# Performance work log

Hardware: AMD Instinct MI355X
Metric: run time of the kernel (lower is better)

The kernel has to match this reference:

```python
import jax, jax.numpy as jnp
import numpy as np

N, F, H, T = 8192, 64, 64, 64   # nodes, fea_hid, gcn_hid, trans_hid
E = 262144                       # edges (avg degree 32)
S, K = 128, 128                  # subgraphs, subgraph size
NEG = 4                          # neg_num


def prelu(x, a):
    return jnp.where(x >= 0, x, a * x)


def setup_inputs() -> dict:
    key = jax.random.key(0)
    ks = jax.random.split(key, 20)
    inp = {}
    inp["feat"] = jax.random.normal(ks[0], (N, F), jnp.float32)
    inp["edge_src"] = jax.random.randint(ks[1], (E,), 0, N)
    inp["edge_dst"] = jax.random.randint(ks[2], (E,), 0, N)
    inp["edge_w"] = jax.random.uniform(ks[3], (E,), jnp.float32)   # normalized adj values
    inp["avg_w"] = jax.random.uniform(ks[4], (E,), jnp.float32)    # adj_avg values
    inp["neg_idx1"] = jax.random.randint(ks[5], (NEG, N), 0, N)
    inp["neg_idx2"] = jax.random.randint(ks[6], (NEG, N), 0, N)
    inp["a_subg_idx"] = jax.random.randint(ks[7], (S, K), 0, N)
    inp["n_subg_idx"] = jax.random.randint(ks[8], (S, K), 0, N)
    inp["a_lap"] = jax.random.normal(ks[9], (S, K, K), jnp.float32) * 0.1
    inp["n_lap"] = jax.random.normal(ks[10], (S, K, K), jnp.float32) * 0.1
    sc = lambda k, sh, d: jax.random.normal(k, sh, jnp.float32) / np.float32(np.sqrt(d))
    inp["W1"] = sc(ks[11], (F, H), F); inp["b1"] = jnp.zeros((H,), jnp.float32)
    inp["W2"] = sc(ks[12], (H, H), H); inp["b2"] = jnp.zeros((H,), jnp.float32)
    inp["Wq"] = sc(ks[13], (H, T), H); inp["bq"] = jnp.zeros((T,), jnp.float32)
    inp["Ws"] = sc(ks[14], (T, 1), T); inp["bs"] = jnp.zeros((1,), jnp.float32)
    inp["B1"] = sc(ks[15], (F, T), F); inp["bd1"] = jnp.zeros((), jnp.float32)
    inp["B2"] = sc(ks[16], (T, H), T); inp["bd2"] = jnp.zeros((), jnp.float32)
    inp["a1"] = jnp.full((), 0.25, jnp.float32)  # PReLU slopes
    inp["a2"] = jnp.full((), 0.25, jnp.float32)
    inp["aq"] = jnp.full((), 0.25, jnp.float32)
    return inp


def _agg(h, src, dst, w):
    # sparse matmul: (sparse adj) @ h via gather + segment_sum
    return jax.ops.segment_sum(w[:, None] * h[src], dst, num_segments=N)


def _forward(feat, edge_w, avg_w, a_lap, n_lap, W1, b1, W2, b2, Wq, bq, Ws, bs,
             B1, bd1, B2, bd2, a1, a2, aq,
             edge_src, edge_dst, neg_idx1, neg_idx2, a_subg_idx, n_subg_idx):
    # GCN 1: fc -> spmm -> +bias -> PReLU ; node_transemb = pre-propagation features
    h1 = feat @ W1                                             # [N,H]  node_transemb
    v1 = prelu(_agg(h1, edge_src, edge_dst, edge_w) + b1, a1)  # [N,H]
    # GCN 2
    h2 = v1 @ W2
    v2 = prelu(_agg(h2, edge_src, edge_dst, edge_w) + b2, a2)
    # transq + PReLU
    node_vec = prelu(v2 @ Wq + bq, aq)                          # [N,T]
    # AvgNeighbor on node_transemb
    node_neighbor = _agg(h1, edge_src, edge_dst, avg_w)         # [N,H]
    # Discriminator 1: bilinear(feat, node_vec); negatives shuffle feat
    p1 = jnp.einsum('nf,ft,nt->n', feat, B1, node_vec) + bd1    # [N]
    n1 = jnp.einsum('knf,ft,nt->kn', feat[neg_idx1], B1, node_vec) + bd1  # [NEG,N]
    # Discriminator 2: bilinear(node_vec, node_neighbor); negatives shuffle node_vec
    p2 = jnp.einsum('nt,th,nh->n', node_vec, B2, node_neighbor) + bd2
    n2 = jnp.einsum('knt,th,nh->kn', node_vec[neg_idx2], B2, node_neighbor) + bd2
    # MIL scores
    score = jax.nn.sigmoid(node_vec @ Ws + bs)[:, 0]            # [N]
    # batched subgraph losses (replaces ragged python loop)
    a_s = score[a_subg_idx]                                     # [S,K]
    n_s = score[n_subg_idx]                                     # [S,K]
    hom = (jnp.einsum('sk,skj,sj->s', a_s, a_lap, a_s)
           + jnp.einsum('sk,skj,sj->s', n_s, n_lap, n_s))       # [S]
    a_sort = -jnp.sort(-a_s, axis=1)                            # descending sort
    n_sort = -jnp.sort(-n_s, axis=1)
    # first position with value below the subgraph mean
    avg_idx = jnp.argmax(a_sort < jnp.mean(a_sort, axis=1, keepdims=True), axis=1)  # [S]
    a_at_avg = jnp.take_along_axis(a_sort, avg_idx[:, None], axis=1)[:, 0]
    ranking_loss = jnp.mean(jax.nn.relu(1.0 - a_sort[:, 0] + n_sort[:, 0]))
    ranking_inner_loss = jnp.mean(jax.nn.relu(1.0 - a_sort[:, 0] + a_at_avg))
    sp_loss = jnp.mean(jnp.sum(a_s, axis=1))
    hom_loss = jnp.sum(hom) / (2.0 * S)
    adj_rebuilt = jax.nn.sigmoid(node_vec @ node_vec.T)         # [N,N]
    return (ranking_loss, ranking_inner_loss, sp_loss, hom_loss, adj_rebuilt,
            p1, n1, p2, n2)


def reference(feat, edge_src, edge_dst, edge_w, avg_w, neg_idx1, neg_idx2,
              a_subg_idx, n_subg_idx, a_lap, n_lap,
              W1, b1, W2, b2, Wq, bq, Ws, bs, B1, bd1, B2, bd2, a1, a2, aq):
    return _forward(feat, edge_w, avg_w, a_lap, n_lap, W1, b1, W2, b2, Wq, bq, Ws, bs,
                    B1, bd1, B2, bd2, a1, a2, aq,
                    edge_src, edge_dst, neg_idx1, neg_idx2, a_subg_idx, n_subg_idx)
```

## Files before the change

### kernel.cpp

```cpp
#include <hip/hip_runtime.h>

#define Nn 8192
#define Ee 262144
#define NEGk 4

#define OFF_H1   0u
#define OFF_M1   524288u
#define OFF_V1   1048576u
#define OFF_NN   1572864u
#define OFF_H2   2097152u
#define OFF_V2   2621440u
#define OFF_NV   3145728u
#define OFF_M2   3670016u
#define OFF_SC   4194304u
#define OFF_PR   4202496u
#define OFF_PI   4202624u
#define OFF_PS   4202752u
#define OFF_PH   4202880u
#define OFF_CNT  4203008u
#define OFF_CUR  4211200u
#define OFF_RS   4219392u
#define OFF_ESRC 4227600u
#define OFF_EW   4489744u
#define OFF_EAW  4751888u
#define OFF_NVH  5014032u
#define OFF_NVL  5276176u
#define OFF_WT   5538320u

using short8 = __attribute__((ext_vector_type(8))) short;
using f32x4  = __attribute__((ext_vector_type(4))) float;

__device__ inline float wave_sum(float v){
  #pragma unroll
  for (int o = 32; o > 0; o >>= 1) v += __shfl_down(v, o, 64);
  return v;
}
__device__ inline float wave_max(float v){
  #pragma unroll
  for (int o = 32; o > 0; o >>= 1) v = fmaxf(v, __shfl_down(v, o, 64));
  return v;
}
__device__ inline unsigned short f2bf(float x){
  unsigned u = __float_as_uint(x);
  unsigned r = (u + 0x7FFFu + ((u >> 16) & 1u)) >> 16;
  return (unsigned short)r;
}
__device__ inline float bf2f(unsigned short h){ return __uint_as_float(((unsigned)h) << 16); }

__global__ __launch_bounds__(256) void zero_k(int* cnt, int* cur){
  int i = blockIdx.x * 256 + threadIdx.x;
  cnt[i] = 0; cur[i] = 0;
}

__global__ __launch_bounds__(256) void hist_k(const int* __restrict__ dst, int* __restrict__ cnt){
  int e = blockIdx.x * 256 + threadIdx.x;
  atomicAdd(&cnt[dst[e]], 1);
}

__global__ __launch_bounds__(256) void scan_k(const int* __restrict__ cnt, int* __restrict__ rs){
  __shared__ int part[256];
  int tid = threadIdx.x;
  int base = tid * 32;
  int local[32]; int s = 0;
  #pragma unroll
  for (int i = 0; i < 32; i++){ local[i] = s; s += cnt[base + i]; }
  part[tid] = s; __syncthreads();
  for (int off = 1; off < 256; off <<= 1){
    int v = (tid >= off) ? part[tid - off] : 0;
    __syncthreads();
    part[tid] += v;
    __syncthreads();
  }
  int ex = part[tid] - s;
  #pragma unroll
  for (int i = 0; i < 32; i++) rs[base + i] = ex + local[i];
  if (tid == 255) rs[Nn] = part[255];
}

__global__ __launch_bounds__(256) void scatter_k(const int* __restrict__ dst, const int* __restrict__ src,
    const float* __restrict__ ew, const float* __restrict__ aw,
    const int* __restrict__ rs, int* __restrict__ cur,
    int* __restrict__ cs, float* __restrict__ cw, float* __restrict__ caw){
  int e = blockIdx.x * 256 + threadIdx.x;
  int d = dst[e];
  int pos = atomicAdd(&cur[d], 1);
  int j = rs[d] + pos;
  cs[j] = src[e]; cw[j] = ew[e]; caw[j] = aw[e];
}

__global__ __launch_bounds__(256) void wtrans_k(const float* __restrict__ W1, const float* __restrict__ B1,
    const float* __restrict__ W2, const float* __restrict__ Wq, const float* __restrict__ B2,
    float* __restrict__ Wt){
  int idx = blockIdx.x * 256 + threadIdx.x;
  int m = idx >> 12, rc = idx & 4095;
  int k = rc >> 6, c = rc & 63;
  const float* src = (m == 0) ? W1 : (m == 1) ? B1 : (m == 2) ? W2 : (m == 3) ? Wq : B2;
  Wt[m * 4096 + c * 64 + k] = src[k * 64 + c];
}

template<bool DUAL, bool EPI, bool BF>
__global__ __launch_bounds__(256) void fc2_k(const float* __restrict__ X,
    const float* __restrict__ WtA, const float* __restrict__ WtB,
    const float* __restrict__ bias, const float* __restrict__ alpha,
    float* __restrict__ Ya, float* __restrict__ Yb,
    unsigned short* __restrict__ hi, unsigned short* __restrict__ lo){
  __shared__ float As[32 * 68];
  int tid = threadIdx.x;
  int r0 = blockIdx.x * 32;
  for (int i = tid; i < 512; i += 256){
    int r = i >> 4, kq = (i & 15) << 2;
    *(float4*)(As + r * 68 + kq) = *(const float4*)(X + (r0 + r) * 64 + kq);
  }
  __syncthreads();
  int tx = tid & 63, wv = tid >> 6;
  float acca[8], accb[8];
  #pragma unroll
  for (int r = 0; r < 8; r++){ acca[r] = 0.f; accb[r] = 0.f; }
  const float* wpa = WtA + tx * 64;
  const float* wpb = DUAL ? (WtB + tx * 64) : WtA;
  #pragma unroll 4
  for (int kq = 0; kq < 64; kq += 4){
    float4 w = *(const float4*)(wpa + kq);
    float4 w2 = *(const float4*)(wpb + kq);
    #pragma unroll
    for (int r = 0; r < 8; r++){
      float4 a = *(const float4*)(As + (wv * 8 + r) * 68 + kq);
      acca[r] += a.x * w.x + a.y * w.y + a.z * w.z + a.w * w.w;
      if (DUAL) accb[r] += a.x * w2.x + a.y * w2.y + a.z * w2.z + a.w * w2.w;
    }
  }
  float al = EPI ? alpha[0] : 0.f;
  float bi = EPI ? bias[tx] : 0.f;
  #pragma unroll
  for (int r = 0; r < 8; r++){
    int row = r0 + wv * 8 + r;
    float x = acca[r];
    if (EPI){ x += bi; x = (x >= 0.f) ? x : al * x; }
    Ya[row * 64 + tx] = x;
    if (BF){
      unsigned short h = f2bf(x);
      hi[row * 64 + tx] = h;
      lo[row * 64 + tx] = f2bf(x - bf2f(h));
    }
    if (DUAL) Yb[row * 64 + tx] = accb[r];
  }
}

template<bool DUAL>
__global__ __launch_bounds__(256) void agg_k(const float* __restrict__ h,
    const int* __restrict__ rs, const int* __restrict__ cs,
    const float* __restrict__ cw, const float* __restrict__ caw,
    const float* __restrict__ bias, const float* __restrict__ alpha,
    float* __restrict__ out1, float* __restrict__ out2){
  int node = (blockIdx.x << 2) + (threadIdx.x >> 6);
  int lane = threadIdx.x & 63;
  int s = rs[node], e = rs[node + 1];
  float acc = 0.f, acc2 = 0.f;
  int i = s;
  for (; i + 4 <= e; i += 4){
    int s0 = cs[i], s1 = cs[i+1], s2 = cs[i+2], s3 = cs[i+3];
    float w0 = cw[i], w1 = cw[i+1], w2 = cw[i+2], w3 = cw[i+3];
    float h0 = h[(s0 << 6) + lane];
    float h1v = h[(s1 << 6) + lane];
    float h2v = h[(s2 << 6) + lane];
    float h3 = h[(s3 << 6) + lane];
    acc += w0 * h0 + w1 * h1v + w2 * h2v + w3 * h3;
    if (DUAL){
      float a0 = caw[i], a1 = caw[i+1], a2 = caw[i+2], a3 = caw[i+3];
      acc2 += a0 * h0 + a1 * h1v + a2 * h2v + a3 * h3;
    }
  }
  for (; i < e; i++){
    int src = cs[i];
    float hv = h[(src << 6) + lane];
    acc += cw[i] * hv;
    if (DUAL) acc2 += caw[i] * hv;
  }
  float x = acc + bias[lane];
  float al = alpha[0];
  out1[(node << 6) + lane] = (x >= 0.f) ? x : al * x;
  if (DUAL) out2[(node << 6) + lane] = acc2;
}

__global__ __launch_bounds__(256) void dots_k(const float* __restrict__ nv,
    const float* __restrict__ M1, const float* __restrict__ M2, const float* __restrict__ nn,
    const float* __restrict__ Wsv, const float* __restrict__ bs,
    const float* __restrict__ bd1, const float* __restrict__ bd2,
    float* __restrict__ p1, float* __restrict__ p2, float* __restrict__ score){
  int node = (blockIdx.x << 2) + (threadIdx.x >> 6);
  int t = threadIdx.x & 63;
  float v = nv[(node << 6) + t];
  float s1 = wave_sum(M1[(node << 6) + t] * v);
  float s2 = wave_sum(M2[(node << 6) + t] * nn[(node << 6) + t]);
  float s3 = wave_sum(v * Wsv[t]);
  if (t == 0){
    p1[node] = s1 + bd1[0];
    p2[node] = s2 + bd2[0];
    score[node] = 1.f / (1.f + __expf(-(s3 + bs[0])));
  }
}

__global__ __launch_bounds__(256) void neg_k(const float* __restrict__ nv,
    const float* __restrict__ M1, const float* __restrict__ M2, const float* __restrict__ nn,
    const int* __restrict__ neg1, const int* __restrict__ neg2,
    const float* __restrict__ bd1, const float* __restrict__ bd2,
    float* __restrict__ n1, float* __restrict__ n2){
  int gid = (blockIdx.x << 2) + (threadIdx.x >> 6);
  int t = threadIdx.x & 63;
  int n = gid & (Nn - 1);
  int i1 = neg1[gid], i2 = neg2[gid];
  float d1 = wave_sum(M1[(i1 << 6) + t] * nv[(n << 6) + t]);
  float d2 = wave_sum(M2[(i2 << 6) + t] * nn[(n << 6) + t]);
  if (t == 0){ n1[gid] = d1 + bd1[0]; n2[gid] = d2 + bd2[0]; }
}

__global__ __launch_bounds__(128) void subg_k(const float* __restrict__ score,
    const int* __restrict__ aidx, const int* __restrict__ nidx,
    const float* __restrict__ alap, const float* __restrict__ nlap,
    float* __restrict__ pr, float* __restrict__ pi, float* __restrict__ ps, float* __restrict__ ph){
  __shared__ float as_[128], ns_[128];
  __shared__ float red[2];
  int s = blockIdx.x, t = threadIdx.x;
  float av = score[aidx[s * 128 + t]];
  float nv = score[nidx[s * 128 + t]];
  as_[t] = av; ns_[t] = nv;
  __syncthreads();
  const float* la = alap + (size_t)s * 16384 + t * 128;
  const float* ln = nlap + (size_t)s * 16384 + t * 128;
  float ya = 0.f, yn = 0.f;
  #pragma unroll 8
  for (int j = 0; j < 128; j += 4){
    float4 wa = *(const float4*)(la + j);
    ya += wa.x * as_[j] + wa.y * as_[j + 1] + wa.z * as_[j + 2] + wa.w * as_[j + 3];
    float4 wn = *(const float4*)(ln + j);
    yn += wn.x * ns_[j] + wn.y * ns_[j + 1] + wn.z * ns_[j + 2] + wn.w * ns_[j + 3];
  }
  float hom = av * ya + nv * yn;
  int wid = t >> 6, lane = t & 63;
  float w;
  w = wave_sum(av);  if (lane == 0) red[wid] = w; __syncthreads();
  float sumA = red[0] + red[1]; __syncthreads();
  w = wave_sum(hom); if (lane == 0) red[wid] = w; __syncthreads();
  float homS = red[0] + red[1]; __syncthreads();
  w = wave_max(av);  if (lane == 0) red[wid] = w; __syncthreads();
  float maxA = fmaxf(red[0], red[1]); __syncthreads();
  w = wave_max(nv);  if (lane == 0) red[wid] = w; __syncthreads();
  float maxN = fmaxf(red[0], red[1]); __syncthreads();
  float mean = sumA * (1.f / 128.f);
  float below = (av < mean) ? av : -3.0e38f;
  w = wave_max(below); if (lane == 0) red[wid] = w; __syncthreads();
  float mb = fmaxf(red[0], red[1]);
  float a_at_avg = (mb < -1.0e37f) ? maxA : mb;
  if (t == 0){
    pr[s] = fmaxf(0.f, 1.f - maxA + maxN);
    pi[s] = fmaxf(0.f, 1.f - maxA + a_at_avg);
    ps[s] = sumA;
    ph[s] = homS;
  }
}

__global__ __launch_bounds__(128) void fin_k(const float* __restrict__ pr, const float* __restrict__ pi,
    const float* __restrict__ ps, const float* __restrict__ ph, float* __restrict__ out){
  __shared__ float red[2];
  int t = threadIdx.x, wid = t >> 6, lane = t & 63;
  float w;
  w = wave_sum(pr[t]); if (lane == 0) red[wid] = w; __syncthreads();
  float sr = red[0] + red[1]; __syncthreads();
  w = wave_sum(pi[t]); if (lane == 0) red[wid] = w; __syncthreads();
  float si = red[0] + red[1]; __syncthreads();
  w = wave_sum(ps[t]); if (lane == 0) red[wid] = w; __syncthreads();
  float ss = red[0] + red[1]; __syncthreads();
  w = wave_sum(ph[t]); if (lane == 0) red[wid] = w; __syncthreads();
  float sh = red[0] + red[1];
  if (t == 0){
    out[0] = sr * (1.f / 128.f);
    out[1] = si * (1.f / 128.f);
    out[2] = ss * (1.f / 128.f);
    out[3] = sh * (1.f / 256.f);
  }
}

__global__ __launch_bounds__(256) void adj_mfma_k(const unsigned short* __restrict__ hi,
    const unsigned short* __restrict__ lo, float* __restrict__ C){
  int tid = threadIdx.x;
  int wave = tid >> 6, lane = tid & 63;
  int quad = lane >> 4, m = lane & 15;
  int rowBase = (blockIdx.y << 7) + ((wave >> 1) << 6);
  int colBase = (blockIdx.x << 7) + ((wave & 1) << 6);

  f32x4 acc[4][4];
  #pragma unroll
  for (int i = 0; i < 4; i++)
    #pragma unroll
    for (int j = 0; j < 4; j++) acc[i][j] = (f32x4){0.f, 0.f, 0.f, 0.f};

  const unsigned short* Ah = hi + ((rowBase + m) << 6) + (quad << 3);
  const unsigned short* Al = lo + ((rowBase + m) << 6) + (quad << 3);
  const unsigned short* Bh = hi + ((colBase + m) << 6) + (quad << 3);
  const unsigned short* Bl = lo + ((colBase + m) << 6) + (quad << 3);

  #pragma unroll
  for (int h = 0; h < 2; h++){
    int ko = h << 5;
    short8 ah[4], al[4], bh[4], bl[4];
    #pragma unroll
    for (int i = 0; i < 4; i++){
      ah[i] = *(const short8*)(Ah + (i << 10) + ko);
      al[i] = *(const short8*)(Al + (i << 10) + ko);
      bh[i] = *(const short8*)(Bh + (i << 10) + ko);
      bl[i] = *(const short8*)(Bl + (i << 10) + ko);
    }
    #pragma unroll
    for (int i = 0; i < 4; i++)
      #pragma unroll
      for (int j = 0; j < 4; j++){
        acc[i][j] = __builtin_amdgcn_mfma_f32_16x16x32_bf16(ah[i], bh[j], acc[i][j], 0, 0, 0);
        acc[i][j] = __builtin_amdgcn_mfma_f32_16x16x32_bf16(ah[i], bl[j], acc[i][j], 0, 0, 0);
        acc[i][j] = __builtin_amdgcn_mfma_f32_16x16x32_bf16(al[i], bh[j], acc[i][j], 0, 0, 0);
      }
  }

  #pragma unroll
  for (int i = 0; i < 4; i++){
    #pragma unroll
    for (int r = 0; r < 4; r++){
      size_t row = (size_t)(rowBase + (i << 4) + (quad << 2) + r);
      float* cp = C + row * Nn + colBase + m;
      #pragma unroll
      for (int j = 0; j < 4; j++){
        float x = acc[i][j][r];
        cp[j << 4] = 1.f / (1.f + __expf(-x));
      }
    }
  }
}

extern "C" void kernel_launch(void* const* d_in, const int* in_sizes, int n_in,
                              void* d_out, int out_size, void* d_ws, size_t ws_size,
                              hipStream_t stream) {
  const float* feat  = (const float*)d_in[0];
  const int*   esrc  = (const int*)d_in[1];
  const int*   edst  = (const int*)d_in[2];
  const float* ewv   = (const float*)d_in[3];
  const float* eawv  = (const float*)d_in[4];
  const int*   neg1  = (const int*)d_in[5];
  const int*   neg2  = (const int*)d_in[6];
  const int*   aidx  = (const int*)d_in[7];
  const int*   nidx  = (const int*)d_in[8];
  const float* alap  = (const float*)d_in[9];
  const float* nlap  = (const float*)d_in[10];
  const float* W1    = (const float*)d_in[11];
  const float* b1    = (const float*)d_in[12];
  const float* W2    = (const float*)d_in[13];
  const float* b2    = (const float*)d_in[14];
  const float* Wq    = (const float*)d_in[15];
  const float* bq    = (const float*)d_in[16];
  const float* Wsv   = (const float*)d_in[17];
  const float* bs    = (const float*)d_in[18];
  const float* B1    = (const float*)d_in[19];
  const float* bd1   = (const float*)d_in[20];
  const float* B2    = (const float*)d_in[21];
  const float* bd2   = (const float*)d_in[22];
  const float* a1    = (const float*)d_in[23];
  const float* a2    = (const float*)d_in[24];
  const float* aq    = (const float*)d_in[25];

  float* ws  = (float*)d_ws;
  float* h1  = ws + OFF_H1;
  float* M1  = ws + OFF_M1;
  float* v1  = ws + OFF_V1;
  float* nn  = ws + OFF_NN;
  float* h2  = ws + OFF_H2;
  float* v2  = ws + OFF_V2;
  float* nv  = ws + OFF_NV;
  float* M2  = ws + OFF_M2;
  float* sc  = ws + OFF_SC;
  float* pr  = ws + OFF_PR;
  float* pi  = ws + OFF_PI;
  float* ps  = ws + OFF_PS;
  float* ph  = ws + OFF_PH;
  int*   cnt = (int*)(ws + OFF_CNT);
  int*   cur = (int*)(ws + OFF_CUR);
  int*   rs  = (int*)(ws + OFF_RS);
  int*   cs  = (int*)(ws + OFF_ESRC);
  float* cw  = ws + OFF_EW;
  float* caw = ws + OFF_EAW;
  unsigned short* nvh = (unsigned short*)(ws + OFF_NVH);
  unsigned short* nvl = (unsigned short*)(ws + OFF_NVL);
  float* Wt  = ws + OFF_WT;
  float* Wt1 = Wt;           float* WtB1 = Wt + 4096;
  float* Wt2 = Wt + 8192;    float* Wtq  = Wt + 12288;
  float* WtB2 = Wt + 16384;

  float* out = (float*)d_out;
  float* adj = out + 4;
  float* p1  = adj + (size_t)Nn * Nn;
  float* n1o = p1 + Nn;
  float* p2  = n1o + NEGk * Nn;
  float* n2o = p2 + Nn;

  zero_k<<<Nn / 256, 256, 0, stream>>>(cnt, cur);
  hist_k<<<Ee / 256, 256, 0, stream>>>(edst, cnt);
  wtrans_k<<<80, 256, 0, stream>>>(W1, B1, W2, Wq, B2, Wt);
  scan_k<<<1, 256, 0, stream>>>(cnt, rs);
  scatter_k<<<Ee / 256, 256, 0, stream>>>(edst, esrc, ewv, eawv, rs, cur, cs, cw, caw);

  fc2_k<true,  false, false><<<Nn / 32, 256, 0, stream>>>(feat, Wt1, WtB1, nullptr, nullptr, h1, M1, nullptr, nullptr);
  agg_k<true ><<<Nn / 4, 256, 0, stream>>>(h1, rs, cs, cw, caw, b1, a1, v1, nn);
  fc2_k<false, false, false><<<Nn / 32, 256, 0, stream>>>(v1, Wt2, nullptr, nullptr, nullptr, h2, nullptr, nullptr, nullptr);
  agg_k<false><<<Nn / 4, 256, 0, stream>>>(h2, rs, cs, cw, caw, b2, a2, v2, nullptr);
  fc2_k<false, true,  true ><<<Nn / 32, 256, 0, stream>>>(v2, Wtq, nullptr, bq, aq, nv, nullptr, nvh, nvl);
  fc2_k<false, false, false><<<Nn / 32, 256, 0, stream>>>(nv, WtB2, nullptr, nullptr, nullptr, M2, nullptr, nullptr, nullptr);

  dots_k<<<Nn / 4, 256, 0, stream>>>(nv, M1, M2, nn, Wsv, bs, bd1, bd2, p1, p2, sc);
  neg_k<<<NEGk * Nn / 4, 256, 0, stream>>>(nv, M1, M2, nn, neg1, neg2, bd1, bd2, n1o, n2o);

  subg_k<<<128, 128, 0, stream>>>(sc, aidx, nidx, alap, nlap, pr, pi, ps, ph);
  fin_k<<<1, 128, 0, stream>>>(pr, pi, ps, ph, out);

  adj_mfma_k<<<dim3(Nn / 128, Nn / 128), 256, 0, stream>>>(nvh, nvl, adj);
}
```

Baseline: 514.3 us.

## Fuse small kernels and make adjacency output stores nontemporal

Merges the zeroing and weight-transpose kernels into one prep kernel, fuses the Wq and B2 projections into a single kernel that keeps nv in shared memory, and combines the positive and negative dot kernels. The subgraph kernel now uses 256 threads with each row split across two threads, and it accumulates the final losses directly with atomics, which removes fin_k. The 256MB sigmoid adjacency write now uses nontemporal stores to avoid cache pollution. Together these cut the number of launches, but the float atomics make the loss sums order-nondeterministic.

```diff
diff --git a/kernel.cpp b/kernel.cpp
--- a/kernel.cpp
+++ b/kernel.cpp
@@ -13,10 +13,6 @@
 #define OFF_NV   3145728u
 #define OFF_M2   3670016u
 #define OFF_SC   4194304u
-#define OFF_PR   4202496u
-#define OFF_PI   4202624u
-#define OFF_PS   4202752u
-#define OFF_PH   4202880u
 #define OFF_CNT  4203008u
 #define OFF_CUR  4211200u
 #define OFF_RS   4219392u
@@ -47,9 +43,22 @@
 }
 __device__ inline float bf2f(unsigned short h){ return __uint_as_float(((unsigned)h) << 16); }
 
-__global__ __launch_bounds__(256) void zero_k(int* cnt, int* cur){
-  int i = blockIdx.x * 256 + threadIdx.x;
-  cnt[i] = 0; cur[i] = 0;
+__global__ __launch_bounds__(256) void prep_k(const float* __restrict__ W1, const float* __restrict__ B1,
+    const float* __restrict__ W2, const float* __restrict__ Wq, const float* __restrict__ B2,
+    float* __restrict__ Wt, int* __restrict__ cnt, int* __restrict__ cur, float* __restrict__ out4){
+  int idx = blockIdx.x * 256 + threadIdx.x;
+  if (idx < 20480){
+    int m = idx >> 12, rc = idx & 4095;
+    int k = rc >> 6, c = rc & 63;
+    const float* src = (m == 0) ? W1 : (m == 1) ? B1 : (m == 2) ? W2 : (m == 3) ? Wq : B2;
+    Wt[m * 4096 + c * 64 + k] = src[k * 64 + c];
+  } else if (idx < 28672){
+    cnt[idx - 20480] = 0;
+  } else if (idx < 36864){
+    cur[idx - 28672] = 0;
+  } else if (idx < 36868){
+    out4[idx - 36864] = 0.f;
+  }
 }
 
 __global__ __launch_bounds__(256) void hist_k(const int* __restrict__ dst, int* __restrict__ cnt){
@@ -88,22 +97,10 @@
   cs[j] = src[e]; cw[j] = ew[e]; caw[j] = aw[e];
 }
 
-__global__ __launch_bounds__(256) void wtrans_k(const float* __restrict__ W1, const float* __restrict__ B1,
-    const float* __restrict__ W2, const float* __restrict__ Wq, const float* __restrict__ B2,
-    float* __restrict__ Wt){
-  int idx = blockIdx.x * 256 + threadIdx.x;
-  int m = idx >> 12, rc = idx & 4095;
-  int k = rc >> 6, c = rc & 63;
-  const float* src = (m == 0) ? W1 : (m == 1) ? B1 : (m == 2) ? W2 : (m == 3) ? Wq : B2;
-  Wt[m * 4096 + c * 64 + k] = src[k * 64 + c];
-}
-
-template<bool DUAL, bool EPI, bool BF>
+template<bool DUAL>
 __global__ __launch_bounds__(256) void fc2_k(const float* __restrict__ X,
     const float* __restrict__ WtA, const float* __restrict__ WtB,
-    const float* __restrict__ bias, const float* __restrict__ alpha,
-    float* __restrict__ Ya, float* __restrict__ Yb,
-    unsigned short* __restrict__ hi, unsigned short* __restrict__ lo){
+    float* __restrict__ Ya, float* __restrict__ Yb){
   __shared__ float As[32 * 68];
   int tid = threadIdx.x;
   int r0 = blockIdx.x * 32;
@@ -129,20 +126,73 @@
       if (DUAL) accb[r] += a.x * w2.x + a.y * w2.y + a.z * w2.z + a.w * w2.w;
     }
   }
-  float al = EPI ? alpha[0] : 0.f;
-  float bi = EPI ? bias[tx] : 0.f;
   #pragma unroll
   for (int r = 0; r < 8; r++){
     int row = r0 + wv * 8 + r;
-    float x = acca[r];
-    if (EPI){ x += bi; x = (x >= 0.f) ? x : al * x; }
-    Ya[row * 64 + tx] = x;
-    if (BF){
-      unsigned short h = f2bf(x);
-      hi[row * 64 + tx] = h;
-      lo[row * 64 + tx] = f2bf(x - bf2f(h));
-    }
+    Ya[row * 64 + tx] = acca[r];
     if (DUAL) Yb[row * 64 + tx] = accb[r];
+  }
+}
+
+__global__ __launch_bounds__(256) void fcq_k(const float* __restrict__ X,
+    const float* __restrict__ Wtq, const float* __restrict__ WtB2,
+    const float* __restrict__ bias, const float* __restrict__ alpha,
+    float* __restrict__ nv, float* __restrict__ M2,
+    unsigned short* __restrict__ hi, unsigned short* __restrict__ lo){
+  __shared__ float As[32 * 68];
+  __shared__ float Ns[32 * 68];
+  int tid = threadIdx.x;
+  int r0 = blockIdx.x * 32;
+  for (int i = tid; i < 512; i += 256){
+    int r = i >> 4, kq = (i & 15) << 2;
+    *(float4*)(As + r * 68 + kq) = *(const float4*)(X + (r0 + r) * 64 + kq);
+  }
+  __syncthreads();
+  int tx = tid & 63, wv = tid >> 6;
+  float acc[8];
+  #pragma unroll
+  for (int r = 0; r < 8; r++) acc[r] = 0.f;
+  const float* wp = Wtq + tx * 64;
+  #pragma unroll 4
+  for (int kq = 0; kq < 64; kq += 4){
+    float4 w = *(const float4*)(wp + kq);
+    #pragma unroll
+    for (int r = 0; r < 8; r++){
+      float4 a = *(const float4*)(As + (wv * 8 + r) * 68 + kq);
+      acc[r] += a.x * w.x + a.y * w.y + a.z * w.z + a.w * w.w;
+    }
+  }
+  float al = alpha[0];
+  float bi = bias[tx];
+  #pragma unroll
+  for (int r = 0; r < 8; r++){
+    int row = r0 + wv * 8 + r;
+    float x = acc[r] + bi;
+    x = (x >= 0.f) ? x : al * x;
+    nv[row * 64 + tx] = x;
+    unsigned short h = f2bf(x);
+    hi[row * 64 + tx] = h;
+    lo[row * 64 + tx] = f2bf(x - bf2f(h));
+    Ns[(wv * 8 + r) * 68 + tx] = x;
+  }
+  __syncthreads();
+  float acc2[8];
+  #pragma unroll
+  for (int r = 0; r < 8; r++) acc2[r] = 0.f;
+  const float* wp2 = WtB2 + tx * 64;
+  #pragma unroll 4
+  for (int kq = 0; kq < 64; kq += 4){
+    float4 w = *(const float4*)(wp2 + kq);
+    #pragma unroll
+    for (int r = 0; r < 8; r++){
+      float4 a = *(const float4*)(Ns + (wv * 8 + r) * 68 + kq);
+      acc2[r] += a.x * w.x + a.y * w.y + a.z * w.z + a.w * w.w;
+    }
+  }
+  #pragma unroll
+  for (int r = 0; r < 8; r++){
+    int row = r0 + wv * 8 + r;
+    M2[row * 64 + tx] = acc2[r];
   }
 }
 
@@ -182,101 +232,89 @@
   if (DUAL) out2[(node << 6) + lane] = acc2;
 }
 
-__global__ __launch_bounds__(256) void dots_k(const float* __restrict__ nv,
+__global__ __launch_bounds__(256) void dotsneg_k(const float* __restrict__ nv,
     const float* __restrict__ M1, const float* __restrict__ M2, const float* __restrict__ nn,
     const float* __restrict__ Wsv, const float* __restrict__ bs,
     const float* __restrict__ bd1, const float* __restrict__ bd2,
-    float* __restrict__ p1, float* __restrict__ p2, float* __restrict__ score){
-  int node = (blockIdx.x << 2) + (threadIdx.x >> 6);
-  int t = threadIdx.x & 63;
-  float v = nv[(node << 6) + t];
-  float s1 = wave_sum(M1[(node << 6) + t] * v);
-  float s2 = wave_sum(M2[(node << 6) + t] * nn[(node << 6) + t]);
-  float s3 = wave_sum(v * Wsv[t]);
-  if (t == 0){
-    p1[node] = s1 + bd1[0];
-    p2[node] = s2 + bd2[0];
-    score[node] = 1.f / (1.f + __expf(-(s3 + bs[0])));
-  }
-}
-
-__global__ __launch_bounds__(256) void neg_k(const float* __restrict__ nv,
-    const float* __restrict__ M1, const float* __restrict__ M2, const float* __restrict__ nn,
     const int* __restrict__ neg1, const int* __restrict__ neg2,
-    const float* __restrict__ bd1, const float* __restrict__ bd2,
+    float* __restrict__ p1, float* __restrict__ p2, float* __restrict__ score,
     float* __restrict__ n1, float* __restrict__ n2){
-  int gid = (blockIdx.x << 2) + (threadIdx.x >> 6);
-  int t = threadIdx.x & 63;
-  int n = gid & (Nn - 1);
-  int i1 = neg1[gid], i2 = neg2[gid];
-  float d1 = wave_sum(M1[(i1 << 6) + t] * nv[(n << 6) + t]);
-  float d2 = wave_sum(M2[(i2 << 6) + t] * nn[(n << 6) + t]);
-  if (t == 0){ n1[gid] = d1 + bd1[0]; n2[gid] = d2 + bd2[0]; }
-}
-
-__global__ __launch_bounds__(128) void subg_k(const float* __restrict__ score,
+  int b = blockIdx.x;
+  int wv = threadIdx.x >> 6, t = threadIdx.x & 63;
+  if (b < (Nn >> 2)){
+    int node = (b << 2) + wv;
+    float v = nv[(node << 6) + t];
+    float s1 = wave_sum(M1[(node << 6) + t] * v);
+    float s2 = wave_sum(M2[(node << 6) + t] * nn[(node << 6) + t]);
+    float s3 = wave_sum(v * Wsv[t]);
+    if (t == 0){
+      p1[node] = s1 + bd1[0];
+      p2[node] = s2 + bd2[0];
+      score[node] = 1.f / (1.f + __expf(-(s3 + bs[0])));
+    }
+  } else {
+    int gid = ((b - (Nn >> 2)) << 2) + wv;
+    int n = gid & (Nn - 1);
+    int i1 = neg1[gid], i2 = neg2[gid];
+    float d1 = wave_sum(M1[(i1 << 6) + t] * nv[(n << 6) + t]);
+    float d2 = wave_sum(M2[(i2 << 6) + t] * nn[(n << 6) + t]);
+    if (t == 0){ n1[gid] = d1 + bd1[0]; n2[gid] = d2 + bd2[0]; }
+  }
+}
+
+__global__ __launch_bounds__(256) void subg_k(const float* __restrict__ score,
     const int* __restrict__ aidx, const int* __restrict__ nidx,
     const float* __restrict__ alap, const float* __restrict__ nlap,
-    float* __restrict__ pr, float* __restrict__ pi, float* __restrict__ ps, float* __restrict__ ph){
+    float* __restrict__ out){
   __shared__ float as_[128], ns_[128];
-  __shared__ float red[2];
+  __shared__ float pya[256], pyn[256];
+  __shared__ float red[4];
   int s = blockIdx.x, t = threadIdx.x;
-  float av = score[aidx[s * 128 + t]];
-  float nv = score[nidx[s * 128 + t]];
-  as_[t] = av; ns_[t] = nv;
+  int r = t >> 1, half = t & 1;
+  if (t < 128){
+    as_[t] = score[aidx[s * 128 + t]];
+    ns_[t] = score[nidx[s * 128 + t]];
+  }
   __syncthreads();
-  const float* la = alap + (size_t)s * 16384 + t * 128;
-  const float* ln = nlap + (size_t)s * 16384 + t * 128;
+  const float* la = alap + (size_t)s * 16384 + r * 128 + half * 64;
+  const float* ln = nlap + (size_t)s * 16384 + r * 128 + half * 64;
   float ya = 0.f, yn = 0.f;
-  #pragma unroll 8
-  for (int j = 0; j < 128; j += 4){
+  #pragma unroll 4
+  for (int j = 0; j < 64; j += 4){
+    int jj = half * 64 + j;
     float4 wa = *(const float4*)(la + j);
-    ya += wa.x * as_[j] + wa.y * as_[j + 1] + wa.z * as_[j + 2] + wa.w * as_[j + 3];
+    ya += wa.x * as_[jj] + wa.y * as_[jj + 1] + wa.z * as_[jj + 2] + wa.w * as_[jj + 3];
     float4 wn = *(const float4*)(ln + j);
-    yn += wn.x * ns_[j] + wn.y * ns_[j + 1] + wn.z * ns_[j + 2] + wn.w * ns_[j + 3];
-  }
-  float hom = av * ya + nv * yn;
+    yn += wn.x * ns_[jj] + wn.y * ns_[jj + 1] + wn.z * ns_[jj + 2] + wn.w * ns_[jj + 3];
+  }
+  pya[t] = ya; pyn[t] = yn;
+  __syncthreads();
   int wid = t >> 6, lane = t & 63;
+  float av = 0.f, nvv = 0.f, hom = 0.f;
+  bool act = (t < 128);
+  if (act){
+    av = as_[t]; nvv = ns_[t];
+    hom = av * (pya[2 * t] + pya[2 * t + 1]) + nvv * (pyn[2 * t] + pyn[2 * t + 1]);
+  }
   float w;
-  w = wave_sum(av);  if (lane == 0) red[wid] = w; __syncthreads();
-  float sumA = red[0] + red[1]; __syncthreads();
+  w = wave_sum(act ? av : 0.f); if (lane == 0) red[wid] = w; __syncthreads();
+  float sumA = red[0] + red[1] + red[2] + red[3]; __syncthreads();
   w = wave_sum(hom); if (lane == 0) red[wid] = w; __syncthreads();
-  float homS = red[0] + red[1]; __syncthreads();
-  w = wave_max(av);  if (lane == 0) red[wid] = w; __syncthreads();
-  float maxA = fmaxf(red[0], red[1]); __syncthreads();
-  w = wave_max(nv);  if (lane == 0) red[wid] = w; __syncthreads();
-  float maxN = fmaxf(red[0], red[1]); __syncthreads();
+  float homS = red[0] + red[1] + red[2] + red[3]; __syncthreads();
+  w = wave_max(act ? av : -3.0e38f); if (lane == 0) red[wid] = w; __syncthreads();
+  float maxA = fmaxf(fmaxf(red[0], red[1]), fmaxf(red[2], red[3])); __syncthreads();
+  w = wave_max(act ? nvv : -3.0e38f); if (lane == 0) red[wid] = w; __syncthreads();
+  float maxN = fmaxf(fmaxf(red[0], red[1]), fmaxf(red[2], red[3])); __syncthreads();
   float mean = sumA * (1.f / 128.f);
-  float below = (av < mean) ? av : -3.0e38f;
+  float below = (act && av < mean) ? av : -3.0e38f;
   w = wave_max(below); if (lane == 0) red[wid] = w; __syncthreads();
-  float mb = fmaxf(red[0], red[1]);
+  float mb = fmaxf(fmaxf(red[0], red[1]), fmaxf(red[2], red[3]));
   float a_at_avg = (mb < -1.0e37f) ? maxA : mb;
   if (t == 0){
-    pr[s] = fmaxf(0.f, 1.f - maxA + maxN);
-    pi[s] = fmaxf(0.f, 1.f - maxA + a_at_avg);
-    ps[s] = sumA;
-    ph[s] = homS;
-  }
-}
-
-__global__ __launch_bounds__(128) void fin_k(const float* __restrict__ pr, const float* __restrict__ pi,
-    const float* __restrict__ ps, const float* __restrict__ ph, float* __restrict__ out){
-  __shared__ float red[2];
-  int t = threadIdx.x, wid = t >> 6, lane = t & 63;
-  float w;
-  w = wave_sum(pr[t]); if (lane == 0) red[wid] = w; __syncthreads();
-  float sr = red[0] + red[1]; __syncthreads();
-  w = wave_sum(pi[t]); if (lane == 0) red[wid] = w; __syncthreads();
-  float si = red[0] + red[1]; __syncthreads();
-  w = wave_sum(ps[t]); if (lane == 0) red[wid] = w; __syncthreads();
-  float ss = red[0] + red[1]; __syncthreads();
-  w = wave_sum(ph[t]); if (lane == 0) red[wid] = w; __syncthreads();
-  float sh = red[0] + red[1];
-  if (t == 0){
-    out[0] = sr * (1.f / 128.f);
-    out[1] = si * (1.f / 128.f);
-    out[2] = ss * (1.f / 128.f);
-    out[3] = sh * (1.f / 256.f);
+    atomicAdd(out + 0, fmaxf(0.f, 1.f - maxA + maxN) * (1.f / 128.f));
+    atomicAdd(out + 1, fmaxf(0.f, 1.f - maxA + a_at_avg) * (1.f / 128.f));
+    atomicAdd(out + 2, sumA * (1.f / 128.f));
+    atomicAdd(out + 3, homS * (1.f / 256.f));
   }
 }
 
@@ -329,7 +367,7 @@
       #pragma unroll
       for (int j = 0; j < 4; j++){
         float x = acc[i][j][r];
-        cp[j << 4] = 1.f / (1.f + __expf(-x));
+        __builtin_nontemporal_store(1.f / (1.f + __expf(-x)), cp + (j << 4));
       }
     }
   }
@@ -375,10 +413,6 @@
   float* nv  = ws + OFF_NV;
   float* M2  = ws + OFF_M2;
   float* sc  = ws + OFF_SC;
-  float* pr  = ws + OFF_PR;
-  float* pi  = ws + OFF_PI;
-  float* ps  = ws + OFF_PS;
-  float* ph  = ws + OFF_PH;
   int*   cnt = (int*)(ws + OFF_CNT);
   int*   cur = (int*)(ws + OFF_CUR);
   int*   rs  = (int*)(ws + OFF_RS);
@@ -399,24 +433,21 @@
   float* p2  = n1o + NEGk * Nn;
   float* n2o = p2 + Nn;
 
-  zero_k<<<Nn / 256, 256, 0, stream>>>(cnt, cur);
+  prep_k<<<145, 256, 0, stream>>>(W1, B1, W2, Wq, B2, Wt, cnt, cur, out);
   hist_k<<<Ee / 256, 256, 0, stream>>>(edst, cnt);
-  wtrans_k<<<80, 256, 0, stream>>>(W1, B1, W2, Wq, B2, Wt);
   scan_k<<<1, 256, 0, stream>>>(cnt, rs);
   scatter_k<<<Ee / 256, 256, 0, stream>>>(edst, esrc, ewv, eawv, rs, cur, cs, cw, caw);
 
-  fc2_k<true,  false, false><<<Nn / 32, 256, 0, stream>>>(feat, Wt1, WtB1, nullptr, nullptr, h1, M1, nullptr, nullptr);
+  fc2_k<true ><<<Nn / 32, 256, 0, stream>>>(feat, Wt1, WtB1, h1, M1);
   agg_k<true ><<<Nn / 4, 256, 0, stream>>>(h1, rs, cs, cw, caw, b1, a1, v1, nn);
-  fc2_k<false, false, false><<<Nn / 32, 256, 0, stream>>>(v1, Wt2, nullptr, nullptr, nullptr, h2, nullptr, nullptr, nullptr);
+  fc2_k<false><<<Nn / 32, 256, 0, stream>>>(v1, Wt2, nullptr, h2, nullptr);
   agg_k<false><<<Nn / 4, 256, 0, stream>>>(h2, rs, cs, cw, caw, b2, a2, v2, nullptr);
-  fc2_k<false, true,  true ><<<Nn / 32, 256, 0, stream>>>(v2, Wtq, nullptr, bq, aq, nv, nullptr, nvh, nvl);
-  fc2_k<false, false, false><<<Nn / 32, 256, 0, stream>>>(nv, WtB2, nullptr, nullptr, nullptr, M2, nullptr, nullptr, nullptr);
-
-  dots_k<<<Nn / 4, 256, 0, stream>>>(nv, M1, M2, nn, Wsv, bs, bd1, bd2, p1, p2, sc);
-  neg_k<<<NEGk * Nn / 4, 256, 0, stream>>>(nv, M1, M2, nn, neg1, neg2, bd1, bd2, n1o, n2o);
-
-  subg_k<<<128, 128, 0, stream>>>(sc, aidx, nidx, alap, nlap, pr, pi, ps, ph);
-  fin_k<<<1, 128, 0, stream>>>(pr, pi, ps, ph, out);
+  fcq_k<<<Nn / 32, 256, 0, stream>>>(v2, Wtq, WtB2, bq, aq, nv, M2, nvh, nvl);
+
+  dotsneg_k<<<(Nn / 4) + (NEGk * Nn / 4), 256, 0, stream>>>(nv, M1, M2, nn, Wsv, bs, bd1, bd2,
+                                                            neg1, neg2, p1, p2, sc, n1o, n2o);
+
+  subg_k<<<128, 256, 0, stream>>>(sc, aidx, nidx, alap, nlap, out);
 
   adj_mfma_k<<<dim3(Nn / 128, Nn / 128), 256, 0, stream>>>(nvh, nvl, adj);
 }
```

New measurement: 551.0 us. 7.1% more time.
